# Kernel optimization log

Measured on AMD Instinct MI355X. Metric: run time of the kernel, lower is better.

The kernel has to match this reference:

```python
import jax, jax.numpy as jnp
import numpy as np

N = 96  # fixed by nn.LayerNorm([96]) in the module
EPS = 1e-6


def _dct2_matrix(n, dtype=jnp.float32):
    # DCT-II with the module's scaling (norm=None, returns 2*V):
    # D[k, i] = 2 * cos(pi * (2i + 1) * k / (2n))
    k = jnp.arange(n, dtype=dtype)[:, None]
    i = jnp.arange(n, dtype=dtype)[None, :]
    return 2.0 * jnp.cos(jnp.pi * (2.0 * i + 1.0) * k / (2.0 * n))


def _layernorm(y, gamma, beta):
    mu = jnp.mean(y, axis=-1, keepdims=True)
    var = jnp.mean(jnp.square(y - mu), axis=-1, keepdims=True)
    return (y - mu) * jax.lax.rsqrt(var + EPS) * gamma + beta


def setup_inputs() -> dict:
    key = jax.random.key(0)
    k1, k2, k3 = jax.random.split(key, 3)
    b, c, l = 512, 1024, N
    x = jax.random.normal(k1, (b, c, l), dtype=jnp.float32)
    # torch Linear default init ~ U(-1/sqrt(fan_in), 1/sqrt(fan_in)); gaussian*scale is fine for a baseline
    W1 = jax.random.normal(k2, (2 * N, N), dtype=jnp.float32) * (1.0 / np.sqrt(N))
    W2 = jax.random.normal(k3, (N, 2 * N), dtype=jnp.float32) * (1.0 / np.sqrt(2 * N))
    ln_gamma = jnp.ones((N,), dtype=jnp.float32)
    ln_beta = jnp.zeros((N,), dtype=jnp.float32)
    return {"x": x, "W1": W1, "W2": W2, "ln_gamma": ln_gamma, "ln_beta": ln_beta}


def reference(x, W1, W2, ln_gamma, ln_beta):
    # x: [b, c, 96]. The per-channel python loop in the original is just a
    # batched DCT-II along the last axis -> single matmul with the DCT matrix.
    D = _dct2_matrix(N, x.dtype)
    stack_dct = jnp.einsum('bcl,kl->bck', x, D)
    lr = _layernorm(stack_dct, ln_gamma, ln_beta)
    h = jax.nn.relu(jnp.einsum('bck,hk->bch', lr, W1))   # Linear(96 -> 192), dropout is identity in eval
    s = jax.nn.sigmoid(jnp.einsum('bch,kh->bck', h, W2))  # Linear(192 -> 96)
    lr_weight = _layernorm(s, ln_gamma, ln_beta)          # same LayerNorm module reused
    return x * lr_weight
```

## Files before the change

### kernel.cpp

```cpp
#include <hip/hip_runtime.h>
#include <math.h>

typedef _Float16 v8h  __attribute__((ext_vector_type(8)));
typedef float    fx4  __attribute__((ext_vector_type(4)));

#define S1_FRAGS 18
#define S2_FRAGS 36
#define S3_FRAGS 36

__global__ void prep_frags(const float* __restrict__ W1,
                           const float* __restrict__ W2,
                           v8h* __restrict__ ws) {
    const int f    = blockIdx.x;
    const int lane = threadIdx.x;
    v8h v;
    if (f < S1_FRAGS) {
        const int t = f / 3, s = f % 3;
        const int n  = t * 16 + (lane & 15);
        const int k0 = s * 32 + (lane >> 4) * 8;
#pragma unroll
        for (int j = 0; j < 8; ++j) {
            const int i = k0 + j;
            const float ang = 3.14159265358979323846f * (float)((2 * i + 1) * n) / 192.0f;
            v[j] = (_Float16)(2.0f * cosf(ang));
        }
    } else if (f < S1_FRAGS + S2_FRAGS) {
        const int g = f - S1_FRAGS;
        const int t = g / 3, s = g % 3;
        const int n  = t * 16 + (lane & 15);
        const int k0 = s * 32 + (lane >> 4) * 8;
#pragma unroll
        for (int j = 0; j < 8; ++j) v[j] = (_Float16)W1[n * 96 + k0 + j];
    } else {
        const int g = f - S1_FRAGS - S2_FRAGS;
        const int t = g / 6, s = g % 6;
        const int n  = t * 16 + (lane & 15);
        const int k0 = s * 32 + (lane >> 4) * 8;
#pragma unroll
        for (int j = 0; j < 8; ++j) v[j] = (_Float16)W2[n * 192 + k0 + j];
    }
    ws[f * 64 + lane] = v;
}

#define LDA 104
#define LDH 200

__global__ __launch_bounds__(256, 3)
void fused_dct_mlp(const float* __restrict__ x,
                   const float* __restrict__ gamma,
                   const float* __restrict__ beta,
                   const v8h* __restrict__ wf,
                   float* __restrict__ out) {
    __shared__ _Float16 LRB[64][LDA];
    __shared__ _Float16 HB[64][LDH];

    const int tid  = threadIdx.x;
    const int lane = tid & 63;
    const int wave = tid >> 6;
    const int m0   = wave * 16;
    const int lr_  = lane & 15;
    const int lk   = lane >> 4;

    const long row0 = (long)blockIdx.x * 64;
    const float* arow = x + (row0 + m0 + lr_) * 96;

    float gv[6], bv[6];
#pragma unroll
    for (int t = 0; t < 6; ++t) {
        gv[t] = gamma[t * 16 + lr_];
        bv[t] = beta[t * 16 + lr_];
    }

    fx4 acc1[6];
#pragma unroll
    for (int t = 0; t < 6; ++t) acc1[t] = (fx4){0.f, 0.f, 0.f, 0.f};
#pragma unroll
    for (int s = 0; s < 3; ++s) {
        const float* ap = arow + s * 32 + lk * 8;
        fx4 a0 = *(const fx4*)ap;
        fx4 a1 = *(const fx4*)(ap + 4);
        v8h a;
#pragma unroll
        for (int j = 0; j < 4; ++j) { a[j] = (_Float16)a0[j]; a[4 + j] = (_Float16)a1[j]; }
#pragma unroll
        for (int t = 0; t < 6; ++t) {
            v8h b = wf[(t * 3 + s) * 64 + lane];
            acc1[t] = __builtin_amdgcn_mfma_f32_16x16x32_f16(a, b, acc1[t], 0, 0, 0);
        }
    }

    {
        float sum[4] = {0, 0, 0, 0}, sq[4] = {0, 0, 0, 0};
#pragma unroll
        for (int t = 0; t < 6; ++t)
#pragma unroll
            for (int r = 0; r < 4; ++r) { float v = acc1[t][r]; sum[r] += v; sq[r] += v * v; }
#pragma unroll
        for (int m = 1; m <= 8; m <<= 1)
#pragma unroll
            for (int r = 0; r < 4; ++r) {
                sum[r] += __shfl_xor(sum[r], m, 64);
                sq[r]  += __shfl_xor(sq[r],  m, 64);
            }
        float mu[4], rs[4];
#pragma unroll
        for (int r = 0; r < 4; ++r) {
            mu[r] = sum[r] * (1.0f / 96.0f);
            float var = sq[r] * (1.0f / 96.0f) - mu[r] * mu[r];
            rs[r] = __builtin_amdgcn_rsqf(var + 1e-6f);
        }
#pragma unroll
        for (int t = 0; t < 6; ++t) {
            const int col = t * 16 + lr_;
#pragma unroll
            for (int r = 0; r < 4; ++r) {
                float w = (acc1[t][r] - mu[r]) * rs[r] * gv[t] + bv[t];
                LRB[m0 + lk * 4 + r][col] = (_Float16)w;
            }
        }
    }

    fx4 acc2[12];
#pragma unroll
    for (int t = 0; t < 12; ++t) acc2[t] = (fx4){0.f, 0.f, 0.f, 0.f};
#pragma unroll
    for (int s = 0; s < 3; ++s) {
        v8h a = *(const v8h*)&LRB[m0 + lr_][s * 32 + lk * 8];
        const v8h* bp = wf + S1_FRAGS * 64;
#pragma unroll
        for (int t = 0; t < 12; ++t) {
            v8h b = bp[(t * 3 + s) * 64 + lane];
            acc2[t] = __builtin_amdgcn_mfma_f32_16x16x32_f16(a, b, acc2[t], 0, 0, 0);
        }
    }
#pragma unroll
    for (int t = 0; t < 12; ++t) {
        const int col = t * 16 + lr_;
#pragma unroll
        for (int r = 0; r < 4; ++r)
            HB[m0 + lk * 4 + r][col] = (_Float16)fmaxf(acc2[t][r], 0.0f);
    }

    fx4 acc3[6];
#pragma unroll
    for (int t = 0; t < 6; ++t) acc3[t] = (fx4){0.f, 0.f, 0.f, 0.f};
#pragma unroll
    for (int s = 0; s < 6; ++s) {
        v8h a = *(const v8h*)&HB[m0 + lr_][s * 32 + lk * 8];
        const v8h* bp = wf + (S1_FRAGS + S2_FRAGS) * 64;
#pragma unroll
        for (int t = 0; t < 6; ++t) {
            v8h b = bp[(t * 6 + s) * 64 + lane];
            acc3[t] = __builtin_amdgcn_mfma_f32_16x16x32_f16(a, b, acc3[t], 0, 0, 0);
        }
    }
#pragma unroll
    for (int t = 0; t < 6; ++t)
#pragma unroll
        for (int r = 0; r < 4; ++r)
            acc3[t][r] = __builtin_amdgcn_rcpf(1.0f + __expf(-acc3[t][r]));

    {
        float sum[4] = {0, 0, 0, 0}, sq[4] = {0, 0, 0, 0};
#pragma unroll
        for (int t = 0; t < 6; ++t)
#pragma unroll
            for (int r = 0; r < 4; ++r) { float v = acc3[t][r]; sum[r] += v; sq[r] += v * v; }
#pragma unroll
        for (int m = 1; m <= 8; m <<= 1)
#pragma unroll
            for (int r = 0; r < 4; ++r) {
                sum[r] += __shfl_xor(sum[r], m, 64);
                sq[r]  += __shfl_xor(sq[r],  m, 64);
            }
        float mu[4], rs[4];
#pragma unroll
        for (int r = 0; r < 4; ++r) {
            mu[r] = sum[r] * (1.0f / 96.0f);
            float var = sq[r] * (1.0f / 96.0f) - mu[r] * mu[r];
            rs[r] = __builtin_amdgcn_rsqf(var + 1e-6f);
        }
#pragma unroll
        for (int t = 0; t < 6; ++t) {
            const int col = t * 16 + lr_;
#pragma unroll
            for (int r = 0; r < 4; ++r) {
                const long grow = row0 + m0 + lk * 4 + r;
                const long off  = grow * 96 + col;
                float w = (acc3[t][r] - mu[r]) * rs[r] * gv[t] + bv[t];
                out[off] = x[off] * w;
            }
        }
    }
}

extern "C" void kernel_launch(void* const* d_in, const int* in_sizes, int n_in,
                              void* d_out, int out_size, void* d_ws, size_t ws_size,
                              hipStream_t stream) {
    const float* x     = (const float*)d_in[0];
    const float* W1    = (const float*)d_in[1];
    const float* W2    = (const float*)d_in[2];
    const float* gamma = (const float*)d_in[3];
    const float* beta  = (const float*)d_in[4];
    float* out = (float*)d_out;
    v8h* ws = (v8h*)d_ws;

    prep_frags<<<S1_FRAGS + S2_FRAGS + S3_FRAGS, 64, 0, stream>>>(W1, W2, ws);

    const long rows = (long)in_sizes[0] / 96;
    fused_dct_mlp<<<(int)(rows / 64), 256, 0, stream>>>(x, gamma, beta, ws, out);
}
```

Baseline: 437.8 us.

## Process two 64-row tiles per block to reuse weight fragment loads

Result: slower. 524.1 us (+19.7%).

```diff
diff --git a/kernel.cpp b/kernel.cpp
--- a/kernel.cpp
+++ b/kernel.cpp
@@ -42,7 +42,6 @@
     ws[f * 64 + lane] = v;
 }
 
-#define LDA 104
 #define LDH 200
 
 __global__ __launch_bounds__(256, 3)
@@ -51,8 +50,7 @@
                    const float* __restrict__ beta,
                    const v8h* __restrict__ wf,
                    float* __restrict__ out) {
-    __shared__ _Float16 LRB[64][LDA];
-    __shared__ _Float16 HB[64][LDH];
+    __shared__ _Float16 SB[2][64][LDH];
 
     const int tid  = threadIdx.x;
     const int lane = tid & 63;
@@ -61,8 +59,7 @@
     const int lr_  = lane & 15;
     const int lk   = lane >> 4;
 
-    const long row0 = (long)blockIdx.x * 64;
-    const float* arow = x + (row0 + m0 + lr_) * 96;
+    const long row0 = (long)blockIdx.x * 128;
 
     float gv[6], bv[6];
 #pragma unroll
@@ -71,30 +68,37 @@
         bv[t] = beta[t * 16 + lr_];
     }
 
-    fx4 acc1[6];
-#pragma unroll
-    for (int t = 0; t < 6; ++t) acc1[t] = (fx4){0.f, 0.f, 0.f, 0.f};
-#pragma unroll
-    for (int s = 0; s < 3; ++s) {
-        const float* ap = arow + s * 32 + lk * 8;
-        fx4 a0 = *(const fx4*)ap;
-        fx4 a1 = *(const fx4*)(ap + 4);
-        v8h a;
-#pragma unroll
-        for (int j = 0; j < 4; ++j) { a[j] = (_Float16)a0[j]; a[4 + j] = (_Float16)a1[j]; }
-#pragma unroll
-        for (int t = 0; t < 6; ++t) {
-            v8h b = wf[(t * 3 + s) * 64 + lane];
-            acc1[t] = __builtin_amdgcn_mfma_f32_16x16x32_f16(a, b, acc1[t], 0, 0, 0);
-        }
-    }
-
-    {
+    fx4 acc1[2][6];
+#pragma unroll
+    for (int u = 0; u < 2; ++u)
+#pragma unroll
+        for (int t = 0; t < 6; ++t) acc1[u][t] = (fx4){0.f, 0.f, 0.f, 0.f};
+#pragma unroll
+    for (int u = 0; u < 2; ++u) {
+        const float* arow = x + (row0 + u * 64 + m0 + lr_) * 96;
+#pragma unroll
+        for (int s = 0; s < 3; ++s) {
+            const float* ap = arow + s * 32 + lk * 8;
+            fx4 a0 = *(const fx4*)ap;
+            fx4 a1 = *(const fx4*)(ap + 4);
+            v8h a;
+#pragma unroll
+            for (int j = 0; j < 4; ++j) { a[j] = (_Float16)a0[j]; a[4 + j] = (_Float16)a1[j]; }
+#pragma unroll
+            for (int t = 0; t < 6; ++t) {
+                v8h b = wf[(t * 3 + s) * 64 + lane];
+                acc1[u][t] = __builtin_amdgcn_mfma_f32_16x16x32_f16(a, b, acc1[u][t], 0, 0, 0);
+            }
+        }
+    }
+
+#pragma unroll
+    for (int u = 0; u < 2; ++u) {
         float sum[4] = {0, 0, 0, 0}, sq[4] = {0, 0, 0, 0};
 #pragma unroll
         for (int t = 0; t < 6; ++t)
 #pragma unroll
-            for (int r = 0; r < 4; ++r) { float v = acc1[t][r]; sum[r] += v; sq[r] += v * v; }
+            for (int r = 0; r < 4; ++r) { float v = acc1[u][t][r]; sum[r] += v; sq[r] += v * v; }
 #pragma unroll
         for (int m = 1; m <= 8; m <<= 1)
 #pragma unroll
@@ -114,58 +118,72 @@
             const int col = t * 16 + lr_;
 #pragma unroll
             for (int r = 0; r < 4; ++r) {
-                float w = (acc1[t][r] - mu[r]) * rs[r] * gv[t] + bv[t];
-                LRB[m0 + lk * 4 + r][col] = (_Float16)w;
-            }
-        }
-    }
-
-    fx4 acc2[12];
-#pragma unroll
-    for (int t = 0; t < 12; ++t) acc2[t] = (fx4){0.f, 0.f, 0.f, 0.f};
-#pragma unroll
-    for (int s = 0; s < 3; ++s) {
-        v8h a = *(const v8h*)&LRB[m0 + lr_][s * 32 + lk * 8];
-        const v8h* bp = wf + S1_FRAGS * 64;
+                float w = (acc1[u][t][r] - mu[r]) * rs[r] * gv[t] + bv[t];
+                SB[u][m0 + lk * 4 + r][col] = (_Float16)w;
+            }
+        }
+    }
+
+    fx4 acc2[2][12];
+#pragma unroll
+    for (int u = 0; u < 2; ++u)
+#pragma unroll
+        for (int t = 0; t < 12; ++t) acc2[u][t] = (fx4){0.f, 0.f, 0.f, 0.f};
+#pragma unroll
+    for (int u = 0; u < 2; ++u)
+#pragma unroll
+        for (int s = 0; s < 3; ++s) {
+            v8h a = *(const v8h*)&SB[u][m0 + lr_][s * 32 + lk * 8];
+            const v8h* bp = wf + S1_FRAGS * 64;
+#pragma unroll
+            for (int t = 0; t < 12; ++t) {
+                v8h b = bp[(t * 3 + s) * 64 + lane];
+                acc2[u][t] = __builtin_amdgcn_mfma_f32_16x16x32_f16(a, b, acc2[u][t], 0, 0, 0);
+            }
+        }
+    asm volatile("" ::: "memory");
+#pragma unroll
+    for (int u = 0; u < 2; ++u)
 #pragma unroll
         for (int t = 0; t < 12; ++t) {
-            v8h b = bp[(t * 3 + s) * 64 + lane];
-            acc2[t] = __builtin_amdgcn_mfma_f32_16x16x32_f16(a, b, acc2[t], 0, 0, 0);
-        }
-    }
-#pragma unroll
-    for (int t = 0; t < 12; ++t) {
-        const int col = t * 16 + lr_;
-#pragma unroll
-        for (int r = 0; r < 4; ++r)
-            HB[m0 + lk * 4 + r][col] = (_Float16)fmaxf(acc2[t][r], 0.0f);
-    }
-
-    fx4 acc3[6];
-#pragma unroll
-    for (int t = 0; t < 6; ++t) acc3[t] = (fx4){0.f, 0.f, 0.f, 0.f};
-#pragma unroll
-    for (int s = 0; s < 6; ++s) {
-        v8h a = *(const v8h*)&HB[m0 + lr_][s * 32 + lk * 8];
-        const v8h* bp = wf + (S1_FRAGS + S2_FRAGS) * 64;
-#pragma unroll
-        for (int t = 0; t < 6; ++t) {
-            v8h b = bp[(t * 6 + s) * 64 + lane];
-            acc3[t] = __builtin_amdgcn_mfma_f32_16x16x32_f16(a, b, acc3[t], 0, 0, 0);
-        }
-    }
-#pragma unroll
-    for (int t = 0; t < 6; ++t)
-#pragma unroll
-        for (int r = 0; r < 4; ++r)
-            acc3[t][r] = __builtin_amdgcn_rcpf(1.0f + __expf(-acc3[t][r]));
-
-    {
+            const int col = t * 16 + lr_;
+#pragma unroll
+            for (int r = 0; r < 4; ++r)
+                SB[u][m0 + lk * 4 + r][col] = (_Float16)fmaxf(acc2[u][t][r], 0.0f);
+        }
+
+    fx4 acc3[2][6];
+#pragma unroll
+    for (int u = 0; u < 2; ++u)
+#pragma unroll
+        for (int t = 0; t < 6; ++t) acc3[u][t] = (fx4){0.f, 0.f, 0.f, 0.f};
+#pragma unroll
+    for (int u = 0; u < 2; ++u)
+#pragma unroll
+        for (int s = 0; s < 6; ++s) {
+            v8h a = *(const v8h*)&SB[u][m0 + lr_][s * 32 + lk * 8];
+            const v8h* bp = wf + (S1_FRAGS + S2_FRAGS) * 64;
+#pragma unroll
+            for (int t = 0; t < 6; ++t) {
+                v8h b = bp[(t * 6 + s) * 64 + lane];
+                acc3[u][t] = __builtin_amdgcn_mfma_f32_16x16x32_f16(a, b, acc3[u][t], 0, 0, 0);
+            }
+        }
+#pragma unroll
+    for (int u = 0; u < 2; ++u)
+#pragma unroll
+        for (int t = 0; t < 6; ++t)
+#pragma unroll
+            for (int r = 0; r < 4; ++r)
+                acc3[u][t][r] = __builtin_amdgcn_rcpf(1.0f + __expf(-acc3[u][t][r]));
+
+#pragma unroll
+    for (int u = 0; u < 2; ++u) {
         float sum[4] = {0, 0, 0, 0}, sq[4] = {0, 0, 0, 0};
 #pragma unroll
         for (int t = 0; t < 6; ++t)
 #pragma unroll
-            for (int r = 0; r < 4; ++r) { float v = acc3[t][r]; sum[r] += v; sq[r] += v * v; }
+            for (int r = 0; r < 4; ++r) { float v = acc3[u][t][r]; sum[r] += v; sq[r] += v * v; }
 #pragma unroll
         for (int m = 1; m <= 8; m <<= 1)
 #pragma unroll
@@ -185,9 +203,9 @@
             const int col = t * 16 + lr_;
 #pragma unroll
             for (int r = 0; r < 4; ++r) {
-                const long grow = row0 + m0 + lk * 4 + r;
+                const long grow = row0 + u * 64 + m0 + lk * 4 + r;
                 const long off  = grow * 96 + col;
-                float w = (acc3[t][r] - mu[r]) * rs[r] * gv[t] + bv[t];
+                float w = (acc3[u][t][r] - mu[r]) * rs[r] * gv[t] + bv[t];
                 out[off] = x[off] * w;
             }
         }
@@ -208,5 +226,5 @@
     prep_frags<<<S1_FRAGS + S2_FRAGS + S3_FRAGS, 64, 0, stream>>>(W1, W2, ws);
 
     const long rows = (long)in_sizes[0] / 96;
-    fused_dct_mlp<<<(int)(rows / 64), 256, 0, stream>>>(x, gamma, beta, ws, out);
+    fused_dct_mlp<<<(int)(rows / 128), 256, 0, stream>>>(x, gamma, beta, ws, out);
 }
```
